# Performance work log

Measured on AMD Instinct MI355X. Metric: run time of the kernel, lower is better.

The kernel has to match this reference:

```python
import jax, jax.numpy as jnp
import numpy as np

N_HEADS = 16
D_MODEL = 1024
D_KV = 64


def setup_inputs() -> dict:
    key = jax.random.key(0)
    ks = jax.random.split(key, 5)
    x = jax.random.normal(ks[0], (4, 2048, D_MODEL), dtype=jnp.float32)
    # per-head projections stacked: [H, D_MODEL, D_KV]
    WQ = jax.random.normal(ks[1], (N_HEADS, D_MODEL, D_KV), dtype=jnp.float32) * (D_MODEL ** -0.5)
    WK = jax.random.normal(ks[2], (N_HEADS, D_MODEL, D_KV), dtype=jnp.float32) * (D_MODEL ** -0.5)
    WV = jax.random.normal(ks[3], (N_HEADS, D_MODEL, D_KV), dtype=jnp.float32) * (D_MODEL ** -0.5)
    WO = jax.random.normal(ks[4], (N_HEADS * D_KV, D_MODEL), dtype=jnp.float32) * ((N_HEADS * D_KV) ** -0.5)
    return {"x": x, "WQ": WQ, "WK": WK, "WV": WV, "WO": WO}


def reference(x, WQ, WK, WV, WO):
    # Batched over heads instead of the original per-head Python loop.
    # q,k,v: [B, H, S, Dk]
    q = jnp.einsum('bsd,hdk->bhsk', x, WQ)
    k = jnp.einsum('bsd,hdk->bhsk', x, WK)
    v = jnp.einsum('bsd,hdk->bhsk', x, WV)
    scale = 1.0 / jnp.sqrt(jnp.asarray(q.shape[-1], q.dtype))
    scores = jnp.einsum('bhqk,bhsk->bhqs', q, k) * scale  # [B, H, S, S]
    attn = jax.nn.softmax(scores, axis=-1)
    o = jnp.einsum('bhqs,bhsk->bhqk', attn, v)            # [B, H, S, Dk]
    # concat heads along feature dim == transpose + reshape
    B, H, S, Dk = o.shape
    o = o.transpose(0, 2, 1, 3).reshape(B, S, H * Dk)
    return o @ WO
```

## Files before the change

### kernel.cpp

```cpp
#include <hip/hip_runtime.h>
#include <stdint.h>
#include <stddef.h>


typedef __attribute__((ext_vector_type(8))) short short8;
typedef __attribute__((ext_vector_type(4))) float floatx4;
typedef __attribute__((ext_vector_type(16))) float floatx16;

#define MFMA_BF16(a, b, c) __builtin_amdgcn_mfma_f32_16x16x32_bf16((a), (b), (c), 0, 0, 0)
#define MFMA32_BF16(a, b, c) __builtin_amdgcn_mfma_f32_32x32x16_bf16((a), (b), (c), 0, 0, 0)

__device__ __forceinline__ unsigned short f32_bf16(float f) {
  union { float f; unsigned u; } v; v.f = f;
  unsigned r = v.u + 0x7fffu + ((v.u >> 16) & 1u);
  return (unsigned short)(r >> 16);
}

__device__ __forceinline__ unsigned pack_bf16_rh(float a, float b) {
  unsigned ua = __float_as_uint(a) + 0x8000u;
  unsigned ub = __float_as_uint(b) + 0x8000u;
  return __builtin_amdgcn_perm(ub, ua, 0x07060302u);
}

__device__ __forceinline__ float fast_exp2(float x) {
#if __has_builtin(__builtin_amdgcn_exp2f)
  return __builtin_amdgcn_exp2f(x);
#else
  return exp2f(x);
#endif
}

__device__ __forceinline__ void g2l16(const void* g, void* l) {
  __builtin_amdgcn_global_load_lds((const __attribute__((address_space(1))) void*)g,
                                   (__attribute__((address_space(3))) void*)l,
                                   16, 0, 0);
}


__global__ __launch_bounds__(256) void cvt_x_k(const float* __restrict__ x,
                                               unsigned short* __restrict__ xb) {
  int i = (blockIdx.x * 256 + threadIdx.x) * 4;
  float4 v = *(const float4*)(x + i);
  ushort4 o;
  o.x = f32_bf16(v.x); o.y = f32_bf16(v.y); o.z = f32_bf16(v.z); o.w = f32_bf16(v.w);
  *(ushort4*)(xb + i) = o;
}

__global__ __launch_bounds__(256) void cvt_wqkv_k(const float* __restrict__ WQ,
                                                  const float* __restrict__ WK,
                                                  const float* __restrict__ WV,
                                                  unsigned short* __restrict__ Wt) {
  int idx = blockIdx.x * 256 + threadIdx.x;
  int n = idx >> 10, d = idx & 1023;
  int typ = n >> 10, rem = n & 1023;
  int h = rem >> 6, dk = rem & 63;
  const float* W = (typ == 0) ? WQ : ((typ == 1) ? WK : WV);
  Wt[idx] = f32_bf16(W[((size_t)h * 1024 + d) * 64 + dk]);
}

__global__ __launch_bounds__(256) void cvt_wo_k(const float* __restrict__ WO,
                                                unsigned short* __restrict__ Wt) {
  int idx = blockIdx.x * 256 + threadIdx.x;
  int n = idx >> 10, k = idx & 1023;
  Wt[idx] = f32_bf16(WO[(size_t)k * 1024 + n]);
}


__global__ __launch_bounds__(256, 2)
void gemm_qkv_k(const unsigned short* __restrict__ A,
                const unsigned short* __restrict__ Bt,
                unsigned short* __restrict__ Qo,
                unsigned short* __restrict__ Ko,
                unsigned short* __restrict__ Vo) {
  __shared__ __align__(16) unsigned short As[8192];
  __shared__ __align__(16) unsigned short Bs[8192];
  const int lane = threadIdx.x & 63;
  const int wave = threadIdx.x >> 6;
  const int quad = lane >> 4;
  const int t = lane & 15;
  const int wm = wave >> 1, wn = wave & 1;
  const int row0 = blockIdx.y * 128;
  const int col0 = blockIdx.x * 128;

  floatx4 acc[4][4];
  #pragma unroll
  for (int i = 0; i < 4; ++i)
    #pragma unroll
    for (int j = 0; j < 4; ++j) acc[i][j] = (floatx4)0.0f;

  for (int k0 = 0; k0 < 1024; k0 += 64) {
    #pragma unroll
    for (int i = 0; i < 4; ++i) {
      int s = (wave * 4 + i) * 64 + lane;
      int r = s >> 3, kc = (s & 7) ^ (r & 7);
      g2l16(A  + (size_t)(row0 + r) * 1024 + k0 + kc * 8, As + (wave * 4 + i) * 512);
      g2l16(Bt + (size_t)(col0 + r) * 1024 + k0 + kc * 8, Bs + (wave * 4 + i) * 512);
    }
    __syncthreads();
    #pragma unroll
    for (int kk = 0; kk < 2; ++kk) {
      short8 af[4], bf[4];
      #pragma unroll
      for (int mt = 0; mt < 4; ++mt) {
        int r = wm * 64 + mt * 16 + t;
        int kc = (kk * 4 + quad) ^ (r & 7);
        af[mt] = *(const short8*)(As + (r * 8 + kc) * 8);
      }
      #pragma unroll
      for (int nt = 0; nt < 4; ++nt) {
        int r = wn * 64 + nt * 16 + t;
        int kc = (kk * 4 + quad) ^ (r & 7);
        bf[nt] = *(const short8*)(Bs + (r * 8 + kc) * 8);
      }
      #pragma unroll
      for (int mt = 0; mt < 4; ++mt)
        #pragma unroll
        for (int nt = 0; nt < 4; ++nt)
          acc[mt][nt] = MFMA_BF16(af[mt], bf[nt], acc[mt][nt]);
    }
    __syncthreads();
  }

  const int typ = col0 >> 10;
  const float qscale = 0.18033688011112042f;
  #pragma unroll
  for (int mt = 0; mt < 4; ++mt) {
    int grow0 = row0 + wm * 64 + mt * 16 + quad * 4;
    int b = grow0 >> 11;
    int s = grow0 & 2047;
    #pragma unroll
    for (int nt = 0; nt < 4; ++nt) {
      int gcol = col0 + wn * 64 + nt * 16 + t;
      int rem = gcol & 1023;
      int h = rem >> 6, dk = rem & 63;
      int bhh = b * 16 + h;
      if (typ == 0) {
        #pragma unroll
        for (int rg = 0; rg < 4; ++rg)
          Qo[((size_t)bhh * 2048 + s + rg) * 64 + dk] = f32_bf16(acc[mt][nt][rg] * qscale);
      } else if (typ == 1) {
        #pragma unroll
        for (int rg = 0; rg < 4; ++rg)
          Ko[((size_t)bhh * 2048 + s + rg) * 64 + dk] = f32_bf16(acc[mt][nt][rg]);
      } else {
        ushort4 pv;
        pv.x = f32_bf16(acc[mt][nt][0]);
        pv.y = f32_bf16(acc[mt][nt][1]);
        pv.z = f32_bf16(acc[mt][nt][2]);
        pv.w = f32_bf16(acc[mt][nt][3]);
        *(ushort4*)(Vo + ((size_t)bhh * 64 + dk) * 2048 + s) = pv;
      }
    }
  }
}


__global__ __launch_bounds__(256, 3)
void attn_k(const unsigned short* __restrict__ Qg_,
            const unsigned short* __restrict__ Kg_,
            const unsigned short* __restrict__ Vg_,
            unsigned short* __restrict__ O) {
  __shared__ __align__(16) char smem[32768];
  const int lane = threadIdx.x & 63;
  const int wave = threadIdx.x >> 6;
  const int h32 = lane >> 5;
  const int c32 = lane & 31;
  const int bh = blockIdx.y;
  const int q0 = blockIdx.x * 128;
  const unsigned short* Qg = Qg_ + ((size_t)bh * 2048 + q0) * 64;
  const unsigned short* Kg = Kg_ + (size_t)bh * 2048 * 64;
  const unsigned short* Vg = Vg_ + (size_t)bh * 64 * 2048;

  #pragma unroll
  for (int i = 0; i < 4; ++i) {
    int s = (wave * 4 + i) * 64 + lane;
    int r = s >> 3, kc = (s & 7) ^ (r & 7);
    g2l16(Qg + (size_t)r * 64 + kc * 8, smem + 16384 + (wave * 4 + i) * 1024);
  }
  __syncthreads();

  short8 qf[4];
  {
    int rq = wave * 32 + c32;
    #pragma unroll
    for (int dc = 0; dc < 4; ++dc) {
      int kc = (dc * 2 + h32) ^ (c32 & 7);
      qf[dc] = *(const short8*)(smem + 16384 + (rq * 8 + kc) * 16);
    }
  }

  floatx16 acc[2];
  acc[0] = (floatx16)0.0f; acc[1] = (floatx16)0.0f;
  float rsp = 0.0f;

  for (int s0 = 0; s0 < 2048; s0 += 64) {
    #pragma unroll
    for (int i = 0; i < 2; ++i) {
      int s = (wave * 2 + i) * 64 + lane;
      int r = s >> 3, kc = (s & 7) ^ (r & 7);
      g2l16(Kg + (size_t)(s0 + r) * 64 + kc * 8, smem + (wave * 2 + i) * 1024);
      g2l16(Vg + (size_t)r * 2048 + s0 + kc * 8, smem + 8192 + (wave * 2 + i) * 1024);
    }
    __syncthreads();

    #pragma unroll
    for (int kb = 0; kb < 2; ++kb) {
      floatx16 sc = (floatx16)0.0f;
      #pragma unroll
      for (int dc = 0; dc < 4; ++dc) {
        int rk = kb * 32 + c32;
        int kc = (dc * 2 + h32) ^ (c32 & 7);
        short8 kf = *(const short8*)(smem + (rk * 8 + kc) * 16);
        sc = MFMA32_BF16(kf, qf[dc], sc);
      }
      float p[16];
      #pragma unroll
      for (int r = 0; r < 16; ++r) { p[r] = fast_exp2(sc[r]); rsp += p[r]; }
      unsigned pk[8];
      #pragma unroll
      for (int i = 0; i < 8; ++i) pk[i] = pack_bf16_rh(p[2 * i], p[2 * i + 1]);
      unsigned x0 = __shfl_xor((int)(h32 ? pk[0] : pk[2]), 32);
      unsigned x1 = __shfl_xor((int)(h32 ? pk[1] : pk[3]), 32);
      unsigned x2 = __shfl_xor((int)(h32 ? pk[4] : pk[6]), 32);
      unsigned x3 = __shfl_xor((int)(h32 ? pk[5] : pk[7]), 32);
      union { unsigned u[4]; short8 s8; } af0, af1;
      af0.u[0] = h32 ? x0 : pk[0];  af0.u[1] = h32 ? x1 : pk[1];
      af0.u[2] = h32 ? pk[2] : x0;  af0.u[3] = h32 ? pk[3] : x1;
      af1.u[0] = h32 ? x2 : pk[4];  af1.u[1] = h32 ? x3 : pk[5];
      af1.u[2] = h32 ? pk[6] : x2;  af1.u[3] = h32 ? pk[7] : x3;
      #pragma unroll
      for (int ksp = 0; ksp < 2; ++ksp) {
        short8 af = ksp ? af1.s8 : af0.s8;
        int cc = kb * 4 + ksp * 2 + h32;
        #pragma unroll
        for (int nb = 0; nb < 2; ++nb) {
          int rv = nb * 32 + c32;
          int kcv = cc ^ (c32 & 7);
          short8 bv = *(const short8*)(smem + 8192 + (rv * 8 + kcv) * 16);
          acc[nb] = MFMA32_BF16(af, bv, acc[nb]);
        }
      }
    }
    __syncthreads();
  }

  float lsum = rsp + __shfl_xor(rsp, 32);

  const int b = bh >> 4, h = bh & 15;
  #pragma unroll
  for (int g = 0; g < 4; ++g) {
    #pragma unroll
    for (int rr = 0; rr < 4; ++rr) {
      int qrel = rr + 8 * g + 4 * h32;
      float rl = 1.0f / __shfl(lsum, qrel);
      int token = b * 2048 + q0 + wave * 32 + qrel;
      size_t base = (size_t)token * 1024 + h * 64;
      O[base + c32]      = f32_bf16(acc[0][4 * g + rr] * rl);
      O[base + 32 + c32] = f32_bf16(acc[1][4 * g + rr] * rl);
    }
  }
}


__global__ __launch_bounds__(256, 2)
void gemm_out_k(const unsigned short* __restrict__ A,
                const unsigned short* __restrict__ Bt,
                float* __restrict__ C) {
  __shared__ __align__(16) unsigned short As[8192];
  __shared__ __align__(16) unsigned short Bs[8192];
  const int lane = threadIdx.x & 63;
  const int wave = threadIdx.x >> 6;
  const int quad = lane >> 4;
  const int t = lane & 15;
  const int wm = wave >> 1, wn = wave & 1;
  const int row0 = blockIdx.y * 128;
  const int col0 = blockIdx.x * 128;

  floatx4 acc[4][4];
  #pragma unroll
  for (int i = 0; i < 4; ++i)
    #pragma unroll
    for (int j = 0; j < 4; ++j) acc[i][j] = (floatx4)0.0f;

  for (int k0 = 0; k0 < 1024; k0 += 64) {
    #pragma unroll
    for (int i = 0; i < 4; ++i) {
      int s = (wave * 4 + i) * 64 + lane;
      int r = s >> 3, kc = (s & 7) ^ (r & 7);
      g2l16(A  + (size_t)(row0 + r) * 1024 + k0 + kc * 8, As + (wave * 4 + i) * 512);
      g2l16(Bt + (size_t)(col0 + r) * 1024 + k0 + kc * 8, Bs + (wave * 4 + i) * 512);
    }
    __syncthreads();
    #pragma unroll
    for (int kk = 0; kk < 2; ++kk) {
      short8 af[4], bf[4];
      #pragma unroll
      for (int mt = 0; mt < 4; ++mt) {
        int r = wm * 64 + mt * 16 + t;
        int kc = (kk * 4 + quad) ^ (r & 7);
        af[mt] = *(const short8*)(As + (r * 8 + kc) * 8);
      }
      #pragma unroll
      for (int nt = 0; nt < 4; ++nt) {
        int r = wn * 64 + nt * 16 + t;
        int kc = (kk * 4 + quad) ^ (r & 7);
        bf[nt] = *(const short8*)(Bs + (r * 8 + kc) * 8);
      }
      #pragma unroll
      for (int mt = 0; mt < 4; ++mt)
        #pragma unroll
        for (int nt = 0; nt < 4; ++nt)
          acc[mt][nt] = MFMA_BF16(af[mt], bf[nt], acc[mt][nt]);
    }
    __syncthreads();
  }

  #pragma unroll
  for (int mt = 0; mt < 4; ++mt) {
    int grow0 = row0 + wm * 64 + mt * 16 + quad * 4;
    #pragma unroll
    for (int nt = 0; nt < 4; ++nt) {
      int gcol = col0 + wn * 64 + nt * 16 + t;
      #pragma unroll
      for (int rg = 0; rg < 4; ++rg)
        C[(size_t)(grow0 + rg) * 1024 + gcol] = acc[mt][nt][rg];
    }
  }
}


extern "C" void kernel_launch(void* const* d_in, const int* in_sizes, int n_in,
                              void* d_out, int out_size, void* d_ws, size_t ws_size,
                              hipStream_t stream) {
  const float* x  = (const float*)d_in[0];
  const float* WQ = (const float*)d_in[1];
  const float* WK = (const float*)d_in[2];
  const float* WV = (const float*)d_in[3];
  const float* WO = (const float*)d_in[4];
  char* ws = (char*)d_ws;
  unsigned short* xb   = (unsigned short*)(ws);
  unsigned short* Wqkv = (unsigned short*)(ws + (size_t)16 * 1024 * 1024);
  unsigned short* WOt  = (unsigned short*)(ws + (size_t)22 * 1024 * 1024);
  unsigned short* Qb   = (unsigned short*)(ws + (size_t)24 * 1024 * 1024);
  unsigned short* Kb   = (unsigned short*)(ws + (size_t)40 * 1024 * 1024);
  unsigned short* Vb   = (unsigned short*)(ws + (size_t)56 * 1024 * 1024);
  float* out = (float*)d_out;

  cvt_x_k<<<8192, 256, 0, stream>>>(x, xb);
  cvt_wqkv_k<<<12288, 256, 0, stream>>>(WQ, WK, WV, Wqkv);
  cvt_wo_k<<<4096, 256, 0, stream>>>(WO, WOt);
  gemm_qkv_k<<<dim3(24, 64), 256, 0, stream>>>(xb, Wqkv, Qb, Kb, Vb);
  attn_k<<<dim3(16, 64), 256, 0, stream>>>(Qb, Kb, Vb, xb );
  gemm_out_k<<<dim3(8, 64), 256, 0, stream>>>(xb, WOt, out);
}
```

Measured before the change: 281.8 us.

## Tile weight transposes through LDS and drop Q staging and P shuffles in attention

Replaces the per-element strided weight conversion kernels with 64x64 LDS-tiled transposes so both the global reads and writes are coalesced. In the attention kernel, Q fragments are now loaded straight from global memory instead of being staged through LDS. This halves the shared-memory footprint and raises the occupancy hint from 3 to 4 blocks. The cross-half lane shuffles of P are removed by reordering how V fragments are read from LDS, using two 8-byte reads per operand instead of one 16-byte read. The trade-off is more, smaller LDS reads and uncoalesced direct Q loads.

Result: faster. 270.1 us (-4.2%).

```diff
diff --git a/kernel.cpp b/kernel.cpp
--- a/kernel.cpp
+++ b/kernel.cpp
@@ -46,23 +46,50 @@
   *(ushort4*)(xb + i) = o;
 }
 
-__global__ __launch_bounds__(256) void cvt_wqkv_k(const float* __restrict__ WQ,
+__global__ __launch_bounds__(256) void cvt_wqkv_t(const float* __restrict__ WQ,
                                                   const float* __restrict__ WK,
                                                   const float* __restrict__ WV,
                                                   unsigned short* __restrict__ Wt) {
-  int idx = blockIdx.x * 256 + threadIdx.x;
-  int n = idx >> 10, d = idx & 1023;
-  int typ = n >> 10, rem = n & 1023;
-  int h = rem >> 6, dk = rem & 63;
+  __shared__ unsigned short tile[64][72];
+  const int th = blockIdx.y;
+  const int typ = th >> 4, h = th & 15;
   const float* W = (typ == 0) ? WQ : ((typ == 1) ? WK : WV);
-  Wt[idx] = f32_bf16(W[((size_t)h * 1024 + d) * 64 + dk]);
-}
-
-__global__ __launch_bounds__(256) void cvt_wo_k(const float* __restrict__ WO,
+  const float* src = W + ((size_t)h * 1024 + blockIdx.x * 64) * 64;
+  const int tid = threadIdx.x;
+  #pragma unroll
+  for (int it = 0; it < 16; ++it) {
+    int f = it * 256 + tid;
+    int dk = f & 63, dl = f >> 6;
+    tile[dk][dl] = f32_bf16(src[(size_t)dl * 64 + dk]);
+  }
+  __syncthreads();
+  unsigned short* dst = Wt + (size_t)(typ * 1024 + h * 64) * 1024 + blockIdx.x * 64;
+  #pragma unroll
+  for (int it = 0; it < 16; ++it) {
+    int f = it * 256 + tid;
+    int d = f & 63, dk = f >> 6;
+    dst[(size_t)dk * 1024 + d] = tile[dk][d];
+  }
+}
+
+__global__ __launch_bounds__(256) void cvt_wo_t(const float* __restrict__ WO,
                                                 unsigned short* __restrict__ Wt) {
-  int idx = blockIdx.x * 256 + threadIdx.x;
-  int n = idx >> 10, k = idx & 1023;
-  Wt[idx] = f32_bf16(WO[(size_t)k * 1024 + n]);
+  __shared__ unsigned short tile[64][72];
+  const int nt = blockIdx.x * 64, kt = blockIdx.y * 64;
+  const int tid = threadIdx.x;
+  #pragma unroll
+  for (int it = 0; it < 16; ++it) {
+    int f = it * 256 + tid;
+    int n = f & 63, kl = f >> 6;
+    tile[n][kl] = f32_bf16(WO[(size_t)(kt + kl) * 1024 + nt + n]);
+  }
+  __syncthreads();
+  #pragma unroll
+  for (int it = 0; it < 16; ++it) {
+    int f = it * 256 + tid;
+    int k = f & 63, nl = f >> 6;
+    Wt[(size_t)(nt + nl) * 1024 + kt + k] = tile[nl][k];
+  }
 }
 
 
@@ -155,12 +182,12 @@
 }
 
 
-__global__ __launch_bounds__(256, 3)
+__global__ __launch_bounds__(256, 4)
 void attn_k(const unsigned short* __restrict__ Qg_,
             const unsigned short* __restrict__ Kg_,
             const unsigned short* __restrict__ Vg_,
             unsigned short* __restrict__ O) {
-  __shared__ __align__(16) char smem[32768];
+  __shared__ __align__(16) char smem[16384];
   const int lane = threadIdx.x & 63;
   const int wave = threadIdx.x >> 6;
   const int h32 = lane >> 5;
@@ -171,22 +198,12 @@
   const unsigned short* Kg = Kg_ + (size_t)bh * 2048 * 64;
   const unsigned short* Vg = Vg_ + (size_t)bh * 64 * 2048;
 
-  #pragma unroll
-  for (int i = 0; i < 4; ++i) {
-    int s = (wave * 4 + i) * 64 + lane;
-    int r = s >> 3, kc = (s & 7) ^ (r & 7);
-    g2l16(Qg + (size_t)r * 64 + kc * 8, smem + 16384 + (wave * 4 + i) * 1024);
-  }
-  __syncthreads();
-
   short8 qf[4];
   {
     int rq = wave * 32 + c32;
     #pragma unroll
-    for (int dc = 0; dc < 4; ++dc) {
-      int kc = (dc * 2 + h32) ^ (c32 & 7);
-      qf[dc] = *(const short8*)(smem + 16384 + (rq * 8 + kc) * 16);
-    }
+    for (int dc = 0; dc < 4; ++dc)
+      qf[dc] = *(const short8*)(Qg + (size_t)rq * 64 + dc * 16 + h32 * 8);
   }
 
   floatx16 acc[2];
@@ -219,25 +236,23 @@
       unsigned pk[8];
       #pragma unroll
       for (int i = 0; i < 8; ++i) pk[i] = pack_bf16_rh(p[2 * i], p[2 * i + 1]);
-      unsigned x0 = __shfl_xor((int)(h32 ? pk[0] : pk[2]), 32);
-      unsigned x1 = __shfl_xor((int)(h32 ? pk[1] : pk[3]), 32);
-      unsigned x2 = __shfl_xor((int)(h32 ? pk[4] : pk[6]), 32);
-      unsigned x3 = __shfl_xor((int)(h32 ? pk[5] : pk[7]), 32);
-      union { unsigned u[4]; short8 s8; } af0, af1;
-      af0.u[0] = h32 ? x0 : pk[0];  af0.u[1] = h32 ? x1 : pk[1];
-      af0.u[2] = h32 ? pk[2] : x0;  af0.u[3] = h32 ? pk[3] : x1;
-      af1.u[0] = h32 ? x2 : pk[4];  af1.u[1] = h32 ? x3 : pk[5];
-      af1.u[2] = h32 ? pk[6] : x2;  af1.u[3] = h32 ? pk[7] : x3;
-      #pragma unroll
-      for (int ksp = 0; ksp < 2; ++ksp) {
-        short8 af = ksp ? af1.s8 : af0.s8;
-        int cc = kb * 4 + ksp * 2 + h32;
+      union { unsigned u[4]; short8 s8; } a0, a1;
+      a0.u[0] = pk[0]; a0.u[1] = pk[1]; a0.u[2] = pk[2]; a0.u[3] = pk[3];
+      a1.u[0] = pk[4]; a1.u[1] = pk[5]; a1.u[2] = pk[6]; a1.u[3] = pk[7];
+      #pragma unroll
+      for (int st = 0; st < 2; ++st) {
+        short8 af = st ? a1.s8 : a0.s8;
+        int c16a = kb * 4 + 2 * st;
+        int c16b = c16a + 1;
         #pragma unroll
         for (int nb = 0; nb < 2; ++nb) {
           int rv = nb * 32 + c32;
-          int kcv = cc ^ (c32 & 7);
-          short8 bv = *(const short8*)(smem + 8192 + (rv * 8 + kcv) * 16);
-          acc[nb] = MFMA32_BF16(af, bv, acc[nb]);
+          const char* vrow = smem + 8192 + rv * 128;
+          uint2 lo = *(const uint2*)(vrow + ((c16a ^ (rv & 7)) * 16) + h32 * 8);
+          uint2 hi = *(const uint2*)(vrow + ((c16b ^ (rv & 7)) * 16) + h32 * 8);
+          union { unsigned u[4]; short8 s8; } bv;
+          bv.u[0] = lo.x; bv.u[1] = lo.y; bv.u[2] = hi.x; bv.u[3] = hi.y;
+          acc[nb] = MFMA32_BF16(af, bv.s8, acc[nb]);
         }
       }
     }
@@ -347,8 +362,8 @@
   float* out = (float*)d_out;
 
   cvt_x_k<<<8192, 256, 0, stream>>>(x, xb);
-  cvt_wqkv_k<<<12288, 256, 0, stream>>>(WQ, WK, WV, Wqkv);
-  cvt_wo_k<<<4096, 256, 0, stream>>>(WO, WOt);
+  cvt_wqkv_t<<<dim3(16, 48), 256, 0, stream>>>(WQ, WK, WV, Wqkv);
+  cvt_wo_t<<<dim3(16, 16), 256, 0, stream>>>(WO, WOt);
   gemm_qkv_k<<<dim3(24, 64), 256, 0, stream>>>(xb, Wqkv, Qb, Kb, Vb);
   attn_k<<<dim3(16, 64), 256, 0, stream>>>(Qb, Kb, Vb, xb );
   gemm_out_k<<<dim3(8, 64), 256, 0, stream>>>(xb, WOt, out);
```
